# Performance work log

Measured on AMD Instinct MI355X. Metric: run time of the kernel, lower is better.

## Reference

```python
import jax, jax.numpy as jnp
import numpy as np

N_NODES = 50000
N_EDGES = 800000
D = 128          # in_feats == out_feats (residual connection)
E_DIMS = 128
NEG_SLOPE = 0.01  # F.leaky_relu default


def setup_inputs() -> dict:
    key = jax.random.key(0)
    ks = jax.random.split(key, 7)
    h = jax.random.normal(ks[0], (N_NODES, D), dtype=jnp.float32)
    edge_w = jax.random.normal(ks[1], (N_EDGES, E_DIMS), dtype=jnp.float32)
    W_self = jax.random.normal(ks[2], (D, D), dtype=jnp.float32) * (2.0 / D) ** 0.5
    W_func = jax.random.normal(ks[3], (D, D), dtype=jnp.float32) * (2.0 / D) ** 0.5
    W_att = jax.random.normal(ks[4], (1, 2 * D + E_DIMS), dtype=jnp.float32) * 0.1
    src = jax.random.randint(ks[5], (N_EDGES,), 0, N_NODES, dtype=jnp.int32)
    dst = jax.random.randint(ks[6], (N_EDGES,), 0, N_NODES, dtype=jnp.int32)
    return {"h": h, "edge_w": edge_w, "W_self": W_self, "W_func": W_func,
            "W_att": W_att, "src": src, "dst": dst}


def reference(h, edge_w, W_self, W_func, W_att, src, dst):
    N = h.shape[0]
    h_in = h
    h_s = h @ W_self.T                     # [N, D] self transform
    z = h @ W_func.T                       # [N, D] message transform

    # attention logit: leaky_relu(W_att @ [z_src, z_dst, e_w]) -- split the
    # single linear into per-node / per-edge pieces (same math, no big concat)
    wa = W_att[0]
    s_src = z @ wa[:D]                     # [N]
    s_dst = z @ wa[D:2 * D]                # [N]
    s_e = edge_w @ wa[2 * D:]              # [E]
    logits = jax.nn.leaky_relu(s_src[src] + s_dst[dst] + s_e, NEG_SLOPE)  # [E]

    # edge softmax grouped by destination node (ragged mailboxes)
    m = jax.ops.segment_max(logits, dst, num_segments=N)
    m = jnp.where(jnp.isfinite(m), m, 0.0)
    ex = jnp.exp(logits - m[dst])
    denom = jax.ops.segment_sum(ex, dst, num_segments=N)
    a = ex / jnp.maximum(denom[dst], 1e-9)                     # [E]

    # weighted scatter-sum of source messages
    agg = jax.ops.segment_sum(a[:, None] * z[src], dst, num_segments=N)  # [N, D]

    # DGL: nodes with zero in-degree keep their original ndata['h']
    deg = jax.ops.segment_sum(jnp.ones_like(logits), dst, num_segments=N)
    h_new = jnp.where(deg[:, None] > 0, h_s + agg, h_in)

    h_new = jax.nn.relu(h_new)             # relu=True
    return h_in + h_new                    # res_connection=True
```

## Files before the change

kernel.cpp:

```cpp
#include <hip/hip_runtime.h>
#include <hip/hip_bf16.h>
#include <math.h>

#define D 128
constexpr int NT = 64;

__global__ __launch_bounds__(256) void node_transform(
    const float* __restrict__ h, const float* __restrict__ Wf,
    const float* __restrict__ Ws, float* __restrict__ z,
    float* __restrict__ hs_out, int N)
{
    __shared__ float tile[NT * D];
    const int t = threadIdx.x;
    const int n0 = blockIdx.x * NT;
    const float* __restrict__ W = (blockIdx.y == 0) ? Wf : Ws;
    float* __restrict__ out = (blockIdx.y == 0) ? z : hs_out;
    const int nvalid = min(NT, N - n0);

    {
        const float4* __restrict__ src4 = (const float4*)(h + (size_t)n0 * D);
        float4* dst4 = (float4*)tile;
        #pragma unroll
        for (int i = 0; i < 8; ++i) {
            int idx = t + i * 256;
            float4 v = make_float4(0.f, 0.f, 0.f, 0.f);
            if ((idx >> 5) < nvalid) v = src4[idx];
            dst4[idx] = v;
        }
    }
    __syncthreads();

    const int oi = t & 63;
    const int q  = t >> 6;
    float acc0[16], acc1[16];
    #pragma unroll
    for (int n = 0; n < 16; ++n) { acc0[n] = 0.f; acc1[n] = 0.f; }

    const float* __restrict__ w0p = W + (size_t)oi * D;
    const float* __restrict__ w1p = W + (size_t)(oi + 64) * D;

    for (int kk = 0; kk < D; kk += 8) {
        float4 w00 = *(const float4*)(w0p + kk);
        float4 w01 = *(const float4*)(w0p + kk + 4);
        float4 w10 = *(const float4*)(w1p + kk);
        float4 w11 = *(const float4*)(w1p + kk + 4);
        #pragma unroll
        for (int n = 0; n < 16; ++n) {
            const float* hp = &tile[(q * 16 + n) * D + kk];
            float4 a = *(const float4*)hp;
            float4 b = *(const float4*)(hp + 4);
            acc0[n] += a.x * w00.x + a.y * w00.y + a.z * w00.z + a.w * w00.w
                     + b.x * w01.x + b.y * w01.y + b.z * w01.z + b.w * w01.w;
            acc1[n] += a.x * w10.x + a.y * w10.y + a.z * w10.z + a.w * w10.w
                     + b.x * w11.x + b.y * w11.y + b.z * w11.z + b.w * w11.w;
        }
    }

    #pragma unroll
    for (int n = 0; n < 16; ++n) {
        int node = q * 16 + n;
        if (node < nvalid) {
            size_t base = (size_t)(n0 + node) * D;
            out[base + oi]      = acc0[n];
            out[base + oi + 64] = acc1[n];
        }
    }
}

__global__ __launch_bounds__(256) void node_scores(
    const float* __restrict__ z, const float* __restrict__ wa,
    float* __restrict__ s_src, float* __restrict__ s_dst, int N)
{
    const int lane = threadIdx.x & 63;
    const int n = blockIdx.x * 4 + (threadIdx.x >> 6);
    if (n >= N) return;
    float2 zv = *(const float2*)(z + (size_t)n * D + 2 * lane);
    float a = zv.x * wa[2 * lane]     + zv.y * wa[2 * lane + 1];
    float b = zv.x * wa[D + 2 * lane] + zv.y * wa[D + 2 * lane + 1];
    #pragma unroll
    for (int off = 32; off > 0; off >>= 1) {
        a += __shfl_xor(a, off, 64);
        b += __shfl_xor(b, off, 64);
    }
    if (lane == 0) { s_src[n] = a; s_dst[n] = b; }
}

__global__ __launch_bounds__(256) void hist_kernel(
    const int* __restrict__ dst, int* __restrict__ deg, int E)
{
    int e = blockIdx.x * blockDim.x + threadIdx.x;
    if (e < E) atomicAdd(deg + dst[e], 1);
}

__global__ __launch_bounds__(256) void scan_block_sums(
    const int* __restrict__ deg, int* __restrict__ bsum, int N)
{
    __shared__ int s[256];
    int i = blockIdx.x * 256 + threadIdx.x;
    s[threadIdx.x] = (i < N) ? deg[i] : 0;
    for (int o = 128; o > 0; o >>= 1) {
        __syncthreads();
        if (threadIdx.x < o) s[threadIdx.x] += s[threadIdx.x + o];
    }
    if (threadIdx.x == 0) bsum[blockIdx.x] = s[0];
}

__global__ __launch_bounds__(256) void scan_bsum(
    const int* __restrict__ bsum, int* __restrict__ boff, int NB)
{
    __shared__ int s[256];
    int t = threadIdx.x;
    int v = (t < NB) ? bsum[t] : 0;
    s[t] = v;
    for (int o = 1; o < 256; o <<= 1) {
        __syncthreads();
        int x = (t >= o) ? s[t - o] : 0;
        __syncthreads();
        s[t] += x;
    }
    __syncthreads();
    if (t < NB) boff[t] = s[t] - v;
}

__global__ __launch_bounds__(256) void scan_final(
    const int* __restrict__ deg, const int* __restrict__ boff,
    int* __restrict__ off, int* __restrict__ cursor, int N)
{
    __shared__ int s[256];
    int t = threadIdx.x;
    int i = blockIdx.x * 256 + t;
    int v = (i < N) ? deg[i] : 0;
    s[t] = v;
    for (int o = 1; o < 256; o <<= 1) {
        __syncthreads();
        int x = (t >= o) ? s[t - o] : 0;
        __syncthreads();
        s[t] += x;
    }
    __syncthreads();
    if (i < N) {
        int ex = boff[blockIdx.x] + s[t] - v;
        off[i] = ex;
        cursor[i] = ex;
    }
}

__global__ __launch_bounds__(256) void edge_matvec(
    const float* __restrict__ edge_w, const float* __restrict__ wa,
    float* __restrict__ s_e, int E)
{
    const int lg = threadIdx.x & 15;
    const int g0 = (blockIdx.x * blockDim.x + threadIdx.x) >> 4;
    const int ng = (gridDim.x * blockDim.x) >> 4;
    const float4* wa4 = (const float4*)(wa + 2 * D);
    const float4 w0 = wa4[2 * lg];
    const float4 w1 = wa4[2 * lg + 1];
    for (int e = g0; e < E; e += ng) {
        const float4* ewp = (const float4*)(edge_w + (size_t)e * D);
        float4 a = ewp[2 * lg];
        float4 b = ewp[2 * lg + 1];
        float p = a.x * w0.x + a.y * w0.y + a.z * w0.z + a.w * w0.w
                + b.x * w1.x + b.y * w1.y + b.z * w1.z + b.w * w1.w;
        p += __shfl_xor(p, 1, 16);
        p += __shfl_xor(p, 2, 16);
        p += __shfl_xor(p, 4, 16);
        p += __shfl_xor(p, 8, 16);
        if (lg == 0) s_e[e] = p;
    }
}

__global__ __launch_bounds__(256) void edge_scatter(
    const int* __restrict__ src, const int* __restrict__ dst,
    const float* __restrict__ s_src, const float* __restrict__ s_dst,
    const float* __restrict__ s_e, int* __restrict__ cursor,
    int* __restrict__ src_s, float* __restrict__ ex_s, int E)
{
    int e = blockIdx.x * blockDim.x + threadIdx.x;
    if (e >= E) return;
    int s = src[e];
    int d = dst[e];
    float logit = s_src[s] + s_dst[d] + s_e[e];
    logit = (logit > 0.f) ? logit : 0.01f * logit;
    float ex = __expf(logit);
    int pos = atomicAdd(cursor + d, 1);
    src_s[pos] = s;
    ex_s[pos]  = ex;
}

__global__ __launch_bounds__(256) void agg_finalize(
    const int* __restrict__ off, const int* __restrict__ deg,
    const int* __restrict__ src_s, const float* __restrict__ ex_s,
    const float* __restrict__ z, const float* __restrict__ h,
    const float* __restrict__ h_s, float* __restrict__ out, int N)
{
    const int lane = threadIdx.x & 63;
    const int n = blockIdx.x * 4 + (threadIdx.x >> 6);
    if (n >= N) return;
    const int b  = off[n];
    const int dg = deg[n];
    float ax = 0.f, ay = 0.f, dsum = 0.f;
    for (int base = 0; base < dg; base += 64) {
        const int cnt = min(64, dg - base);
        const int idx = b + base + ((lane < cnt) ? lane : 0);
        int   sv = src_s[idx];
        float ev = ex_s[idx];
        for (int j = 0; j < cnt; ++j) {
            int   s  = __shfl(sv, j, 64);
            float ex = __shfl(ev, j, 64);
            dsum += ex;
            float2 zv = *(const float2*)(z + (size_t)s * D + 2 * lane);
            ax += ex * zv.x;
            ay += ex * zv.y;
        }
    }
    float2 hv = *(const float2*)(h + (size_t)n * D + 2 * lane);
    float rx, ry;
    if (dg > 0) {
        float inv = 1.f / fmaxf(dsum, 1e-9f);
        float2 hs = *(const float2*)(h_s + (size_t)n * D + 2 * lane);
        rx = hs.x + ax * inv;
        ry = hs.y + ay * inv;
    } else {
        rx = hv.x; ry = hv.y;
    }
    rx = fmaxf(rx, 0.f); ry = fmaxf(ry, 0.f);
    float2 o = make_float2(hv.x + rx, hv.y + ry);
    *(float2*)(out + (size_t)n * D + 2 * lane) = o;
}

extern "C" void kernel_launch(void* const* d_in, const int* in_sizes, int n_in,
                              void* d_out, int out_size, void* d_ws, size_t ws_size,
                              hipStream_t stream)
{
    const float* h      = (const float*)d_in[0];
    const float* edge_w = (const float*)d_in[1];
    const float* W_self = (const float*)d_in[2];
    const float* W_func = (const float*)d_in[3];
    const float* W_att  = (const float*)d_in[4];
    const int*   src    = (const int*)d_in[5];
    const int*   dst    = (const int*)d_in[6];
    float* out = (float*)d_out;

    const int N = in_sizes[0] / D;
    const int E = in_sizes[1] / D;
    const int NB = (N + 255) / 256;

    float* z     = (float*)d_ws;
    float* ex_s  = z + (size_t)N * D;
    float* s_e   = ex_s + E;
    float* s_src = s_e + E;
    float* s_dst = s_src + N;
    int*   src_s = (int*)(s_dst + N);
    int*   deg   = src_s + E;
    int*   off   = deg + N;
    int*   cursor= off + N;
    int*   bsum  = cursor + N;
    int*   boff  = bsum + 256;

    hipMemsetAsync(deg, 0, (size_t)N * sizeof(int), stream);

    {
        dim3 grid((N + NT - 1) / NT, 2);
        node_transform<<<grid, 256, 0, stream>>>(h, W_func, W_self, z, out, N);
    }
    node_scores<<<(N + 3) / 4, 256, 0, stream>>>(z, W_att, s_src, s_dst, N);

    edge_matvec<<<2048, 256, 0, stream>>>(edge_w, W_att, s_e, E);

    hist_kernel<<<(E + 255) / 256, 256, 0, stream>>>(dst, deg, E);
    scan_block_sums<<<NB, 256, 0, stream>>>(deg, bsum, N);
    scan_bsum<<<1, 256, 0, stream>>>(bsum, boff, NB);
    scan_final<<<NB, 256, 0, stream>>>(deg, boff, off, cursor, N);

    edge_scatter<<<(E + 255) / 256, 256, 0, stream>>>(src, dst, s_src, s_dst,
                                                      s_e, cursor, src_s, ex_s, E);

    agg_finalize<<<(N + 3) / 4, 256, 0, stream>>>(off, deg, src_s, ex_s,
                                                  z, h, out, out, N);
}
```

Measured before the change: 813.8 us.

## Fuse histogram into edge matvec, pack edge buckets, batch gathers, retile GEMM

The degree histogram is folded into the edge-score matvec kernel, which removes one kernel launch and one extra read of dst. Source index and exp weight are packed into a single int2 bucket array, so each edge is written and read with one access instead of two. The aggregation loop now loads 8 bucket entries and their 8 z rows up front before accumulating, in place of per-edge shuffles, so more gather loads are in flight at once. The node transform is retiled to 8 nodes by 4 outputs per thread, which changes the register and LDS reuse pattern.

After: 794.1 us. 2.4% less time.

```diff
diff --git a/kernel.cpp b/kernel.cpp
--- a/kernel.cpp
+++ b/kernel.cpp
@@ -30,39 +30,44 @@
     }
     __syncthreads();
 
-    const int oi = t & 63;
-    const int q  = t >> 6;
-    float acc0[16], acc1[16];
+    const int oi = t & 31;
+    const int q  = t >> 5;
+    float acc[8][4];
     #pragma unroll
-    for (int n = 0; n < 16; ++n) { acc0[n] = 0.f; acc1[n] = 0.f; }
-
-    const float* __restrict__ w0p = W + (size_t)oi * D;
-    const float* __restrict__ w1p = W + (size_t)(oi + 64) * D;
+    for (int n = 0; n < 8; ++n)
+        #pragma unroll
+        for (int m = 0; m < 4; ++m) acc[n][m] = 0.f;
 
     for (int kk = 0; kk < D; kk += 8) {
-        float4 w00 = *(const float4*)(w0p + kk);
-        float4 w01 = *(const float4*)(w0p + kk + 4);
-        float4 w10 = *(const float4*)(w1p + kk);
-        float4 w11 = *(const float4*)(w1p + kk + 4);
-        #pragma unroll
-        for (int n = 0; n < 16; ++n) {
-            const float* hp = &tile[(q * 16 + n) * D + kk];
+        float4 w[4][2];
+        #pragma unroll
+        for (int m = 0; m < 4; ++m) {
+            const float* wr = W + (size_t)(oi + 32 * m) * D + kk;
+            w[m][0] = *(const float4*)wr;
+            w[m][1] = *(const float4*)(wr + 4);
+        }
+        #pragma unroll
+        for (int n = 0; n < 8; ++n) {
+            const float* hp = &tile[(q * 8 + n) * D + kk];
             float4 a = *(const float4*)hp;
             float4 b = *(const float4*)(hp + 4);
-            acc0[n] += a.x * w00.x + a.y * w00.y + a.z * w00.z + a.w * w00.w
-                     + b.x * w01.x + b.y * w01.y + b.z * w01.z + b.w * w01.w;
-            acc1[n] += a.x * w10.x + a.y * w10.y + a.z * w10.z + a.w * w10.w
-                     + b.x * w11.x + b.y * w11.y + b.z * w11.z + b.w * w11.w;
+            #pragma unroll
+            for (int m = 0; m < 4; ++m) {
+                acc[n][m] += a.x * w[m][0].x + a.y * w[m][0].y
+                           + a.z * w[m][0].z + a.w * w[m][0].w
+                           + b.x * w[m][1].x + b.y * w[m][1].y
+                           + b.z * w[m][1].z + b.w * w[m][1].w;
+            }
         }
     }
 
     #pragma unroll
-    for (int n = 0; n < 16; ++n) {
-        int node = q * 16 + n;
+    for (int n = 0; n < 8; ++n) {
+        int node = q * 8 + n;
         if (node < nvalid) {
-            size_t base = (size_t)(n0 + node) * D;
-            out[base + oi]      = acc0[n];
-            out[base + oi + 64] = acc1[n];
+            float* op = out + (size_t)(n0 + node) * D + oi;
+            #pragma unroll
+            for (int m = 0; m < 4; ++m) op[32 * m] = acc[n][m];
         }
     }
 }
@@ -85,69 +90,10 @@
     if (lane == 0) { s_src[n] = a; s_dst[n] = b; }
 }
 
-__global__ __launch_bounds__(256) void hist_kernel(
-    const int* __restrict__ dst, int* __restrict__ deg, int E)
-{
-    int e = blockIdx.x * blockDim.x + threadIdx.x;
-    if (e < E) atomicAdd(deg + dst[e], 1);
-}
-
-__global__ __launch_bounds__(256) void scan_block_sums(
-    const int* __restrict__ deg, int* __restrict__ bsum, int N)
-{
-    __shared__ int s[256];
-    int i = blockIdx.x * 256 + threadIdx.x;
-    s[threadIdx.x] = (i < N) ? deg[i] : 0;
-    for (int o = 128; o > 0; o >>= 1) {
-        __syncthreads();
-        if (threadIdx.x < o) s[threadIdx.x] += s[threadIdx.x + o];
-    }
-    if (threadIdx.x == 0) bsum[blockIdx.x] = s[0];
-}
-
-__global__ __launch_bounds__(256) void scan_bsum(
-    const int* __restrict__ bsum, int* __restrict__ boff, int NB)
-{
-    __shared__ int s[256];
-    int t = threadIdx.x;
-    int v = (t < NB) ? bsum[t] : 0;
-    s[t] = v;
-    for (int o = 1; o < 256; o <<= 1) {
-        __syncthreads();
-        int x = (t >= o) ? s[t - o] : 0;
-        __syncthreads();
-        s[t] += x;
-    }
-    __syncthreads();
-    if (t < NB) boff[t] = s[t] - v;
-}
-
-__global__ __launch_bounds__(256) void scan_final(
-    const int* __restrict__ deg, const int* __restrict__ boff,
-    int* __restrict__ off, int* __restrict__ cursor, int N)
-{
-    __shared__ int s[256];
-    int t = threadIdx.x;
-    int i = blockIdx.x * 256 + t;
-    int v = (i < N) ? deg[i] : 0;
-    s[t] = v;
-    for (int o = 1; o < 256; o <<= 1) {
-        __syncthreads();
-        int x = (t >= o) ? s[t - o] : 0;
-        __syncthreads();
-        s[t] += x;
-    }
-    __syncthreads();
-    if (i < N) {
-        int ex = boff[blockIdx.x] + s[t] - v;
-        off[i] = ex;
-        cursor[i] = ex;
-    }
-}
-
-__global__ __launch_bounds__(256) void edge_matvec(
+__global__ __launch_bounds__(256) void edge_matvec_hist(
     const float* __restrict__ edge_w, const float* __restrict__ wa,
-    float* __restrict__ s_e, int E)
+    const int* __restrict__ dst, float* __restrict__ s_e,
+    int* __restrict__ deg, int E)
 {
     const int lg = threadIdx.x & 15;
     const int g0 = (blockIdx.x * blockDim.x + threadIdx.x) >> 4;
@@ -165,7 +111,63 @@
         p += __shfl_xor(p, 2, 16);
         p += __shfl_xor(p, 4, 16);
         p += __shfl_xor(p, 8, 16);
-        if (lg == 0) s_e[e] = p;
+        if (lg == 0) {
+            s_e[e] = p;
+            atomicAdd(deg + dst[e], 1);
+        }
+    }
+}
+
+__global__ __launch_bounds__(256) void scan_block_sums(
+    const int* __restrict__ deg, int* __restrict__ bsum, int N)
+{
+    __shared__ int s[256];
+    int i = blockIdx.x * 256 + threadIdx.x;
+    s[threadIdx.x] = (i < N) ? deg[i] : 0;
+    for (int o = 128; o > 0; o >>= 1) {
+        __syncthreads();
+        if (threadIdx.x < o) s[threadIdx.x] += s[threadIdx.x + o];
+    }
+    if (threadIdx.x == 0) bsum[blockIdx.x] = s[0];
+}
+
+__global__ __launch_bounds__(256) void scan_bsum(
+    const int* __restrict__ bsum, int* __restrict__ boff, int NB)
+{
+    __shared__ int s[256];
+    int t = threadIdx.x;
+    int v = (t < NB) ? bsum[t] : 0;
+    s[t] = v;
+    for (int o = 1; o < 256; o <<= 1) {
+        __syncthreads();
+        int x = (t >= o) ? s[t - o] : 0;
+        __syncthreads();
+        s[t] += x;
+    }
+    __syncthreads();
+    if (t < NB) boff[t] = s[t] - v;
+}
+
+__global__ __launch_bounds__(256) void scan_final(
+    const int* __restrict__ deg, const int* __restrict__ boff,
+    int* __restrict__ off, int* __restrict__ cursor, int N)
+{
+    __shared__ int s[256];
+    int t = threadIdx.x;
+    int i = blockIdx.x * 256 + t;
+    int v = (i < N) ? deg[i] : 0;
+    s[t] = v;
+    for (int o = 1; o < 256; o <<= 1) {
+        __syncthreads();
+        int x = (t >= o) ? s[t - o] : 0;
+        __syncthreads();
+        s[t] += x;
+    }
+    __syncthreads();
+    if (i < N) {
+        int ex = boff[blockIdx.x] + s[t] - v;
+        off[i] = ex;
+        cursor[i] = ex;
     }
 }
 
@@ -173,7 +175,7 @@
     const int* __restrict__ src, const int* __restrict__ dst,
     const float* __restrict__ s_src, const float* __restrict__ s_dst,
     const float* __restrict__ s_e, int* __restrict__ cursor,
-    int* __restrict__ src_s, float* __restrict__ ex_s, int E)
+    int2* __restrict__ bkt, int E)
 {
     int e = blockIdx.x * blockDim.x + threadIdx.x;
     if (e >= E) return;
@@ -183,15 +185,14 @@
     logit = (logit > 0.f) ? logit : 0.01f * logit;
     float ex = __expf(logit);
     int pos = atomicAdd(cursor + d, 1);
-    src_s[pos] = s;
-    ex_s[pos]  = ex;
+    bkt[pos] = make_int2(s, __float_as_int(ex));
 }
 
 __global__ __launch_bounds__(256) void agg_finalize(
     const int* __restrict__ off, const int* __restrict__ deg,
-    const int* __restrict__ src_s, const float* __restrict__ ex_s,
-    const float* __restrict__ z, const float* __restrict__ h,
-    const float* __restrict__ h_s, float* __restrict__ out, int N)
+    const int2* __restrict__ bkt, const float* __restrict__ z,
+    const float* __restrict__ h, const float* __restrict__ h_s,
+    float* __restrict__ out, int N)
 {
     const int lane = threadIdx.x & 63;
     const int n = blockIdx.x * 4 + (threadIdx.x >> 6);
@@ -199,19 +200,30 @@
     const int b  = off[n];
     const int dg = deg[n];
     float ax = 0.f, ay = 0.f, dsum = 0.f;
-    for (int base = 0; base < dg; base += 64) {
-        const int cnt = min(64, dg - base);
-        const int idx = b + base + ((lane < cnt) ? lane : 0);
-        int   sv = src_s[idx];
-        float ev = ex_s[idx];
-        for (int j = 0; j < cnt; ++j) {
-            int   s  = __shfl(sv, j, 64);
-            float ex = __shfl(ev, j, 64);
+    int e = 0;
+    for (; e + 8 <= dg; e += 8) {
+        int2 p[8];
+        #pragma unroll
+        for (int j = 0; j < 8; ++j) p[j] = bkt[b + e + j];
+        float2 zv[8];
+        #pragma unroll
+        for (int j = 0; j < 8; ++j)
+            zv[j] = *(const float2*)(z + (size_t)p[j].x * D + 2 * lane);
+        #pragma unroll
+        for (int j = 0; j < 8; ++j) {
+            float ex = __int_as_float(p[j].y);
             dsum += ex;
-            float2 zv = *(const float2*)(z + (size_t)s * D + 2 * lane);
-            ax += ex * zv.x;
-            ay += ex * zv.y;
-        }
+            ax += ex * zv[j].x;
+            ay += ex * zv[j].y;
+        }
+    }
+    for (; e < dg; ++e) {
+        int2 p = bkt[b + e];
+        float ex = __int_as_float(p.y);
+        float2 zv = *(const float2*)(z + (size_t)p.x * D + 2 * lane);
+        dsum += ex;
+        ax += ex * zv.x;
+        ay += ex * zv.y;
     }
     float2 hv = *(const float2*)(h + (size_t)n * D + 2 * lane);
     float rx, ry;
@@ -246,12 +258,11 @@
     const int NB = (N + 255) / 256;
 
     float* z     = (float*)d_ws;
-    float* ex_s  = z + (size_t)N * D;
-    float* s_e   = ex_s + E;
+    float* s_e   = z + (size_t)N * D;
     float* s_src = s_e + E;
     float* s_dst = s_src + N;
-    int*   src_s = (int*)(s_dst + N);
-    int*   deg   = src_s + E;
+    int2*  bkt   = (int2*)(s_dst + N);
+    int*   deg   = (int*)(bkt + E);
     int*   off   = deg + N;
     int*   cursor= off + N;
     int*   bsum  = cursor + N;
@@ -265,16 +276,14 @@
     }
     node_scores<<<(N + 3) / 4, 256, 0, stream>>>(z, W_att, s_src, s_dst, N);
 
-    edge_matvec<<<2048, 256, 0, stream>>>(edge_w, W_att, s_e, E);
-
-    hist_kernel<<<(E + 255) / 256, 256, 0, stream>>>(dst, deg, E);
+    edge_matvec_hist<<<2048, 256, 0, stream>>>(edge_w, W_att, dst, s_e, deg, E);
+
     scan_block_sums<<<NB, 256, 0, stream>>>(deg, bsum, N);
     scan_bsum<<<1, 256, 0, stream>>>(bsum, boff, NB);
     scan_final<<<NB, 256, 0, stream>>>(deg, boff, off, cursor, N);
 
     edge_scatter<<<(E + 255) / 256, 256, 0, stream>>>(src, dst, s_src, s_dst,
-                                                      s_e, cursor, src_s, ex_s, E);
-
-    agg_finalize<<<(N + 3) / 4, 256, 0, stream>>>(off, deg, src_s, ex_s,
-                                                  z, h, out, out, N);
-}
+                                                      s_e, cursor, bkt, E);
+
+    agg_finalize<<<(N + 3) / 4, 256, 0, stream>>>(off, deg, bkt, z, h, out, out, N);
+}
```
